# Kernel optimization log

Hardware: AMD Instinct MI355X
Metric: run time of the kernel (lower is better)

Reference implementation:

```python
import jax, jax.numpy as jnp
import numpy as np

N_NODES = 50000
N_EDGES = 800000
IN_DIM = 256
HID = 64
HEADS = 4
OUT_DIM = 16
N_GRAPHS = 64
NEG_SLOPE = 0.2


def setup_inputs() -> dict:
    key = jax.random.key(0)
    ks = jax.random.split(key, 16)
    H2 = HID // 2  # conv2 out channels (heads=1, concat=False)
    H4 = HID // 4
    inp = {
        "x": jax.random.normal(ks[0], (N_NODES, IN_DIM), jnp.float32),
        "edge_index": jax.random.randint(ks[1], (2, N_EDGES), 0, N_NODES, jnp.int64),
        "batch": jnp.sort(jax.random.randint(ks[2], (N_NODES,), 0, N_GRAPHS, jnp.int64)),
        # GATConv 1: in=IN_DIM, out=HID, heads=HEADS, concat=True
        "W1": jax.random.normal(ks[3], (IN_DIM, HEADS * HID), jnp.float32) * 0.05,
        "att_src1": jax.random.normal(ks[4], (HEADS, HID), jnp.float32) * 0.1,
        "att_dst1": jax.random.normal(ks[5], (HEADS, HID), jnp.float32) * 0.1,
        "b1": jnp.zeros((HEADS * HID,), jnp.float32),
        # GATConv 2: in=HEADS*HID, out=HID/2, heads=1, concat=False
        "W2": jax.random.normal(ks[6], (HEADS * HID, H2), jnp.float32) * 0.05,
        "att_src2": jax.random.normal(ks[7], (1, H2), jnp.float32) * 0.1,
        "att_dst2": jax.random.normal(ks[8], (1, H2), jnp.float32) * 0.1,
        "b2": jnp.zeros((H2,), jnp.float32),
        "fc1_w": jax.random.normal(ks[9], (H2, H4), jnp.float32) * 0.1,
        "fc1_b": jnp.zeros((H4,), jnp.float32),
        "fc2_w": jax.random.normal(ks[10], (H4, OUT_DIM), jnp.float32) * 0.1,
        "fc2_b": jnp.zeros((OUT_DIM,), jnp.float32),
    }
    return inp


def gat_conv(x, W, att_src, att_dst, bias, src, dst, num_nodes, concat):
    """PyG-style GATConv (eval mode, self-loops already in src/dst)."""
    H, C = att_src.shape
    h = (x @ W).reshape(num_nodes, H, C)          # [N,H,C]
    a_src = (h * att_src).sum(-1)                 # [N,H]
    a_dst = (h * att_dst).sum(-1)                 # [N,H]
    e = jax.nn.leaky_relu(a_src[src] + a_dst[dst], NEG_SLOPE)  # [E,H]
    # segment softmax over destination nodes (self-loops => every segment nonempty)
    emax = jax.ops.segment_max(e, dst, num_segments=num_nodes)
    ex = jnp.exp(e - emax[dst])
    denom = jax.ops.segment_sum(ex, dst, num_segments=num_nodes)
    alpha = ex / (denom[dst] + 1e-16)             # [E,H]
    msg = h[src] * alpha[:, :, None]              # [E,H,C]
    out = jax.ops.segment_sum(msg, dst, num_segments=num_nodes)  # [N,H,C]
    out = out.reshape(num_nodes, H * C) if concat else out.mean(axis=1)
    return out + bias


def reference(x, edge_index, batch, W1, att_src1, att_dst1, b1,
              W2, att_src2, att_dst2, b2, fc1_w, fc1_b, fc2_w, fc2_b):
    num_nodes = x.shape[0]
    loops = jnp.arange(num_nodes, dtype=edge_index.dtype)
    src = jnp.concatenate([edge_index[0], loops])
    dst = jnp.concatenate([edge_index[1], loops])

    h = gat_conv(x, W1, att_src1, att_dst1, b1, src, dst, num_nodes, concat=True)
    h = jax.nn.relu(h)                                 # dropout: eval no-op
    h = gat_conv(h, W2, att_src2, att_dst2, b2, src, dst, num_nodes, concat=False)

    # global mean pool over graphs
    sums = jax.ops.segment_sum(h, batch, num_segments=N_GRAPHS)
    cnts = jax.ops.segment_sum(jnp.ones((num_nodes,), h.dtype), batch, num_segments=N_GRAPHS)
    g = sums / jnp.maximum(cnts, 1.0)[:, None]         # [G, HID/2]

    g = jax.nn.relu(g)
    g = jax.nn.relu(g @ fc1_w + fc1_b)
    g = jax.nn.relu(g @ fc2_w + fc2_b)
    return g
```

## Files before the change

kernel.cpp:

```cpp
#include <hip/hip_runtime.h>
#include <math.h>

#define NEG 0.2f
#define LMAX 1024
#define CAP 1600
typedef unsigned short u16;
typedef unsigned int u32;
typedef __bf16 bf16x8 __attribute__((ext_vector_type(8)));
typedef float f32x4 __attribute__((ext_vector_type(4)));

__device__ __forceinline__ float bf2f(u16 u) {
    union { unsigned i; float f; } x; x.i = ((unsigned)u) << 16; return x.f;
}
__device__ __forceinline__ u16 f2bf(float f) {
    union { float f; unsigned u; } x; x.f = f;
    unsigned r = x.u + 0x7fffu + ((x.u >> 16) & 1u);
    return (u16)(r >> 16);
}

__global__ __launch_bounds__(256) void bkt_scatter_pad(const int* __restrict__ ei,
                                                       int* __restrict__ bktcur,
                                                       u32* __restrict__ ebuf,
                                                       int E, int ET, int NBK) {
    __shared__ int lcnt[LMAX];
    __shared__ int lbase[LMAX];
    int t = threadIdx.x;
    for (int b = t; b < NBK; b += 256) lcnt[b] = 0;
    __syncthreads();
    int base = blockIdx.x * 8192;
    for (int k = 0; k < 32; ++k) {
        int i = base + k * 256 + t;
        if (i < ET) {
            int d = (i < E) ? ei[E + i] : (i - E);
            atomicAdd(&lcnt[d >> 6], 1);
        }
    }
    __syncthreads();
    for (int b = t; b < NBK; b += 256) {
        int c = lcnt[b];
        lbase[b] = c ? (b * CAP + atomicAdd(&bktcur[b], c)) : 0;
    }
    __syncthreads();
    for (int b = t; b < NBK; b += 256) lcnt[b] = 0;
    __syncthreads();
    for (int k = 0; k < 32; ++k) {
        int i = base + k * 256 + t;
        if (i < ET) {
            int s, d;
            if (i < E) { s = ei[i]; d = ei[E + i]; }
            else       { s = i - E; d = s; }
            int b = d >> 6;
            int idx = atomicAdd(&lcnt[b], 1);
            ebuf[lbase[b] + idx] = (u32)s | ((u32)(d & 63) << 16);
        }
    }
}

__global__ __launch_bounds__(256) void bucket_csr_pad(const u32* __restrict__ ebuf,
                                                      const int* __restrict__ bktcur,
                                                      int* __restrict__ row_ptr,
                                                      int* __restrict__ rowend,
                                                      int* __restrict__ col, int N) {
    __shared__ int cnt[64];
    __shared__ int cur[64];
    int b = blockIdx.x, t = threadIdx.x;
    int v0 = b << 6;
    int s0 = b * CAP, s1 = s0 + bktcur[b];
    if (t < 64) cnt[t] = 0;
    __syncthreads();
    for (int i = s0 + t; i < s1; i += 256)
        atomicAdd(&cnt[(ebuf[i] >> 16) & 63], 1);
    __syncthreads();
    if (t < 64) {
        int c = cnt[t];
        int val = c;
#pragma unroll
        for (int off = 1; off < 64; off <<= 1) {
            int n = __shfl_up(val, off, 64);
            if (t >= off) val += n;
        }
        int excl = s0 + val - c;
        if (v0 + t < N) { row_ptr[v0 + t] = excl; rowend[v0 + t] = excl + c; }
        cur[t] = excl;
    }
    __syncthreads();
    for (int i = s0 + t; i < s1; i += 256) {
        u32 v = ebuf[i];
        int pos = atomicAdd(&cur[(v >> 16) & 63], 1);
        col[pos] = (int)(v & 0xFFFFu);
    }
}

__global__ void prep_all(const float* __restrict__ W1, const float* __restrict__ att_s1,
                         const float* __restrict__ att_d1, u16* __restrict__ w1x,
                         const float* __restrict__ W2, const float* __restrict__ att_s2,
                         const float* __restrict__ att_d2, u16* __restrict__ w2x,
                         int* __restrict__ bktcur, int NBK) {
    int t = threadIdx.x;
    if (blockIdx.x < 256) {
        int k = blockIdx.x;
        int c = t;
        float w = W1[k * 256 + c];
        w1x[c * 256 + k] = f2bf(w);
        int head = c >> 6;
        float vs = w * att_s1[c];
        float vd = w * att_d1[c];
#pragma unroll
        for (int mask = 1; mask < 64; mask <<= 1) {
            vs += __shfl_xor(vs, mask, 64);
            vd += __shfl_xor(vd, mask, 64);
        }
        if ((c & 63) == 0) {
            w1x[(256 + head) * 256 + k] = f2bf(vs);
            w1x[(260 + head) * 256 + k] = f2bf(vd);
            w1x[(264 + head) * 256 + k] = 0;
            w1x[(268 + head) * 256 + k] = 0;
        }
    } else {
        int k = t;
        float a_s = 0.f, a_d = 0.f;
#pragma unroll
        for (int j = 0; j < 32; ++j) {
            float w = W2[k * 32 + j];
            w2x[j * 256 + k] = f2bf(w);
            a_s += w * att_s2[j];
            a_d += w * att_d2[j];
        }
        w2x[32 * 256 + k] = f2bf(a_s);
        w2x[33 * 256 + k] = f2bf(a_d);
#pragma unroll
        for (int r = 34; r < 48; ++r) w2x[r * 256 + k] = 0;
        for (int i = t; i < NBK; i += 256) bktcur[i] = 0;
    }
}

__global__ __launch_bounds__(512) void gemm1_regw(const float* __restrict__ x,
                                                  const u16* __restrict__ w1x,
                                                  u16* __restrict__ h1b,
                                                  float* __restrict__ asad, int N) {
    __shared__ __align__(16) u16 xs[2][16][264];
    int t = threadIdx.x;
    int wave = t >> 6, lane = t & 63;
    int g = lane >> 4, l15 = lane & 15;

    bf16x8 wreg[3][8];
#pragma unroll
    for (int ci = 0; ci < 3; ++ci) {
        int ct = (ci == 2) ? 16 : (wave * 2 + ci);
        const u16* wp = w1x + (size_t)(ct * 16 + l15) * 256 + g * 8;
#pragma unroll
        for (int ks = 0; ks < 8; ++ks)
            wreg[ci][ks] = *reinterpret_cast<const bf16x8*>(wp + ks * 32);
    }

    int srow = t >> 5, sseg = t & 31;
    int ntiles = (N + 15) >> 4;
    int tile0 = blockIdx.x;
    if (tile0 >= ntiles) return;

    auto stage_load = [&](int tile, float4& a0, float4& a1) {
        int arow = tile * 16 + srow; if (arow > N - 1) arow = N - 1;
        const float* xp = x + (size_t)arow * 256 + sseg * 8;
        a0 = *reinterpret_cast<const float4*>(xp);
        a1 = *reinterpret_cast<const float4*>(xp + 4);
    };
    auto stage_write = [&](int buf, const float4& a0, const float4& a1) {
        uint4 o;
        o.x = (unsigned)f2bf(a0.x) | ((unsigned)f2bf(a0.y) << 16);
        o.y = (unsigned)f2bf(a0.z) | ((unsigned)f2bf(a0.w) << 16);
        o.z = (unsigned)f2bf(a1.x) | ((unsigned)f2bf(a1.y) << 16);
        o.w = (unsigned)f2bf(a1.z) | ((unsigned)f2bf(a1.w) << 16);
        *reinterpret_cast<uint4*>(&xs[buf][srow][sseg * 8]) = o;
    };

    {
        float4 a0, a1;
        stage_load(tile0, a0, a1);
        stage_write(0, a0, a1);
    }
    __syncthreads();

    int cur = 0;
    for (int tile = tile0; tile < ntiles; tile += 256) {
        int nxt = tile + 256;
        bool hasnext = nxt < ntiles;
        float4 p0, p1;
        if (hasnext) stage_load(nxt, p0, p1);

        f32x4 acc[3];
#pragma unroll
        for (int ci = 0; ci < 3; ++ci) acc[ci] = (f32x4){0.f, 0.f, 0.f, 0.f};
#pragma unroll
        for (int ks = 0; ks < 8; ++ks) {
            bf16x8 bfr = *reinterpret_cast<const bf16x8*>(&xs[cur][l15][ks * 32 + g * 8]);
#pragma unroll
            for (int ci = 0; ci < 3; ++ci)
                acc[ci] = __builtin_amdgcn_mfma_f32_16x16x32_bf16(wreg[ci][ks], bfr, acc[ci], 0, 0, 0);
        }

        int nrow = tile * 16 + l15;
        if (nrow < N) {
#pragma unroll
            for (int ci = 0; ci < 2; ++ci) {
                int ct = wave * 2 + ci;
                ushort4 o;
                o.x = f2bf(acc[ci][0]); o.y = f2bf(acc[ci][1]);
                o.z = f2bf(acc[ci][2]); o.w = f2bf(acc[ci][3]);
                *reinterpret_cast<ushort4*>(h1b + (size_t)nrow * 256 + ct * 16 + g * 4) = o;
            }
            if (wave == 0 && g < 2) {
#pragma unroll
                for (int reg = 0; reg < 4; ++reg)
                    asad[(size_t)nrow * 8 + g * 4 + reg] = acc[2][reg];
            }
        }
        __syncthreads();
        if (hasnext) stage_write(cur ^ 1, p0, p1);
        __syncthreads();
        cur ^= 1;
    }
}

__global__ __launch_bounds__(256) void conv1_fused(const u16* __restrict__ h1b,
                                                   const float* __restrict__ asad,
                                                   const int* __restrict__ row_ptr,
                                                   const int* __restrict__ rowend,
                                                   const int* __restrict__ col,
                                                   const float* __restrict__ b1,
                                                   u16* __restrict__ hin2b, int N) {
    __shared__ float la[4][128][4];
    __shared__ int   lc[4][128];
    int idx = blockIdx.x * blockDim.x + threadIdx.x;
    int v = idx >> 6; if (v > N - 1) v = N - 1;
    int lane = idx & 63;
    int node = threadIdx.x >> 6;
    int head = lane >> 4, l15 = lane & 15;
    float adst = asad[(size_t)v * 8 + 4 + head];
    int beg = row_ptr[v], end = rowend[v];
    int deg = end - beg;
    bool fast = (deg <= 128);
    float m = -1e30f, l = 0.f;
    if (fast) {
        float e[8]; int u[8];
#pragma unroll
        for (int i = 0; i < 8; ++i) {
            int p = beg + l15 + i * 16;
            float ev = -1e30f; int uu = 0;
            if (p < end) {
                uu = col[p];
                float tv = asad[(size_t)uu * 8 + head] + adst;
                ev = tv > 0.f ? tv : NEG * tv;
            }
            e[i] = ev; u[i] = uu;
        }
        m = e[0];
#pragma unroll
        for (int i = 1; i < 8; ++i) m = fmaxf(m, e[i]);
#pragma unroll
        for (int mask = 1; mask < 16; mask <<= 1) m = fmaxf(m, __shfl_xor(m, mask, 64));
#pragma unroll
        for (int i = 0; i < 8; ++i) {
            int j = l15 + i * 16;
            if (beg + j < end) {
                float a = __expf(e[i] - m);
                l += a;
                la[node][j][head] = a;
                if (head == 0) lc[node][j] = u[i];
            }
        }
#pragma unroll
        for (int mask = 1; mask < 16; mask <<= 1) l += __shfl_xor(l, mask, 64);
    } else {
        for (int p = beg + l15; p < end; p += 16) {
            float tv = asad[(size_t)col[p] * 8 + head] + adst;
            tv = tv > 0.f ? tv : NEG * tv;
            m = fmaxf(m, tv);
        }
#pragma unroll
        for (int mask = 1; mask < 16; mask <<= 1) m = fmaxf(m, __shfl_xor(m, mask, 64));
        for (int p = beg + l15; p < end; p += 16) {
            float tv = asad[(size_t)col[p] * 8 + head] + adst;
            tv = tv > 0.f ? tv : NEG * tv;
            l += __expf(tv - m);
        }
#pragma unroll
        for (int mask = 1; mask < 16; mask <<= 1) l += __shfl_xor(l, mask, 64);
    }
    __syncthreads();
    float inv = 1.f / (l + 1e-16f);

    float ax = 0.f, ay = 0.f, az = 0.f, aw = 0.f;
    if (fast) {
        int j = 0;
        for (; j + 3 < deg; j += 4) {
            float a0 = la[node][j + 0][head];
            float a1 = la[node][j + 1][head];
            float a2 = la[node][j + 2][head];
            float a3 = la[node][j + 3][head];
            int u0 = lc[node][j + 0], u1 = lc[node][j + 1];
            int u2 = lc[node][j + 2], u3 = lc[node][j + 3];
            ushort4 h0 = *reinterpret_cast<const ushort4*>(h1b + (size_t)u0 * 256 + lane * 4);
            ushort4 h1 = *reinterpret_cast<const ushort4*>(h1b + (size_t)u1 * 256 + lane * 4);
            ushort4 h2 = *reinterpret_cast<const ushort4*>(h1b + (size_t)u2 * 256 + lane * 4);
            ushort4 h3 = *reinterpret_cast<const ushort4*>(h1b + (size_t)u3 * 256 + lane * 4);
            ax += a0 * bf2f(h0.x) + a1 * bf2f(h1.x) + a2 * bf2f(h2.x) + a3 * bf2f(h3.x);
            ay += a0 * bf2f(h0.y) + a1 * bf2f(h1.y) + a2 * bf2f(h2.y) + a3 * bf2f(h3.y);
            az += a0 * bf2f(h0.z) + a1 * bf2f(h1.z) + a2 * bf2f(h2.z) + a3 * bf2f(h3.z);
            aw += a0 * bf2f(h0.w) + a1 * bf2f(h1.w) + a2 * bf2f(h2.w) + a3 * bf2f(h3.w);
        }
        for (; j < deg; ++j) {
            float a = la[node][j][head];
            int u = lc[node][j];
            ushort4 hv = *reinterpret_cast<const ushort4*>(h1b + (size_t)u * 256 + lane * 4);
            ax += a * bf2f(hv.x);
            ay += a * bf2f(hv.y);
            az += a * bf2f(hv.z);
            aw += a * bf2f(hv.w);
        }
    } else {
        for (int p = beg; p < end; ++p) {
            int u = col[p];
            float tv = asad[(size_t)u * 8 + head] + adst;
            tv = tv > 0.f ? tv : NEG * tv;
            float a = __expf(tv - m);
            ushort4 hv = *reinterpret_cast<const ushort4*>(h1b + (size_t)u * 256 + lane * 4);
            ax += a * bf2f(hv.x);
            ay += a * bf2f(hv.y);
            az += a * bf2f(hv.z);
            aw += a * bf2f(hv.w);
        }
    }
    int c = lane * 4;
    ushort4 o;
    o.x = f2bf(fmaxf(ax * inv + b1[c + 0], 0.f));
    o.y = f2bf(fmaxf(ay * inv + b1[c + 1], 0.f));
    o.z = f2bf(fmaxf(az * inv + b1[c + 2], 0.f));
    o.w = f2bf(fmaxf(aw * inv + b1[c + 3], 0.f));
    *reinterpret_cast<ushort4*>(hin2b + (size_t)v * 256 + c) = o;
}

__global__ __launch_bounds__(512) void gemm2_mfma(const u16* __restrict__ hin2b,
                                                  const u16* __restrict__ w2x,
                                                  u16* __restrict__ h2b,
                                                  float* __restrict__ as2,
                                                  float* __restrict__ ad2, int N) {
    __shared__ __align__(16) u16 wl[48 * 264];
    for (int f = threadIdx.x; f < 48 * 32; f += 512) {
        int r = f >> 5, cc = f & 31;
        *reinterpret_cast<uint4*>(&wl[r * 264 + cc * 8]) =
            *reinterpret_cast<const uint4*>(w2x + r * 256 + cc * 8);
    }
    __syncthreads();

    int wave = threadIdx.x >> 6, lane = threadIdx.x & 63;
    int g = lane >> 4, l15 = lane & 15;
    int ntiles = (N + 15) >> 4;
    for (int tile = blockIdx.x * 8 + wave; tile < ntiles; tile += gridDim.x * 8) {
        int r0 = tile << 4;
        int arow = r0 + l15; if (arow > N - 1) arow = N - 1;
        const u16* hp = hin2b + (size_t)arow * 256 + g * 8;

        f32x4 acc[3];
#pragma unroll
        for (int n = 0; n < 3; ++n) acc[n] = (f32x4){0.f, 0.f, 0.f, 0.f};

#pragma unroll
        for (int ks = 0; ks < 8; ++ks) {
            bf16x8 af = *reinterpret_cast<const bf16x8*>(hp + ks * 32);
#pragma unroll
            for (int n = 0; n < 3; ++n) {
                bf16x8 bf = *reinterpret_cast<const bf16x8*>(&wl[(n * 16 + l15) * 264 + ks * 32 + g * 8]);
                acc[n] = __builtin_amdgcn_mfma_f32_16x16x32_bf16(af, bf, acc[n], 0, 0, 0);
            }
        }

#pragma unroll
        for (int reg = 0; reg < 4; ++reg) {
            int grow = r0 + g * 4 + reg;
            if (grow < N) {
                h2b[(size_t)grow * 32 + l15]      = f2bf(acc[0][reg]);
                h2b[(size_t)grow * 32 + 16 + l15] = f2bf(acc[1][reg]);
                if (l15 == 0) as2[grow] = acc[2][reg];
                if (l15 == 1) ad2[grow] = acc[2][reg];
            }
        }
    }
}

__global__ __launch_bounds__(256) void conv2_fused(const u16* __restrict__ h2b,
                                                   const float* __restrict__ as2,
                                                   const float* __restrict__ ad2,
                                                   const int* __restrict__ row_ptr,
                                                   const int* __restrict__ rowend,
                                                   const int* __restrict__ col,
                                                   const float* __restrict__ b2,
                                                   float* __restrict__ out2, int N) {
    __shared__ float la[8][128];
    __shared__ int   lc[8][128];
    int idx = blockIdx.x * blockDim.x + threadIdx.x;
    int v = idx >> 5; if (v > N - 1) v = N - 1;
    int lane = idx & 31;
    int node = threadIdx.x >> 5;
    float adst = ad2[v];
    int beg = row_ptr[v], end = rowend[v];
    int deg = end - beg;
    bool fast = (deg <= 128);
    float m = -1e30f, l = 0.f;
    if (fast) {
        float e[4]; int u[4];
#pragma unroll
        for (int i = 0; i < 4; ++i) {
            int p = beg + lane + i * 32;
            float ev = -1e30f; int uu = 0;
            if (p < end) {
                uu = col[p];
                float tv = as2[uu] + adst;
                ev = tv > 0.f ? tv : NEG * tv;
            }
            e[i] = ev; u[i] = uu;
        }
        m = fmaxf(fmaxf(e[0], e[1]), fmaxf(e[2], e[3]));
#pragma unroll
        for (int mask = 1; mask < 32; mask <<= 1) m = fmaxf(m, __shfl_xor(m, mask, 64));
#pragma unroll
        for (int i = 0; i < 4; ++i) {
            int j = lane + i * 32;
            if (beg + j < end) {
                float a = __expf(e[i] - m);
                l += a;
                la[node][j] = a;
                lc[node][j] = u[i];
            }
        }
#pragma unroll
        for (int mask = 1; mask < 32; mask <<= 1) l += __shfl_xor(l, mask, 64);
    } else {
        for (int p = beg + lane; p < end; p += 32) {
            float tv = as2[col[p]] + adst;
            tv = tv > 0.f ? tv : NEG * tv;
            m = fmaxf(m, tv);
        }
#pragma unroll
        for (int mask = 1; mask < 32; mask <<= 1) m = fmaxf(m, __shfl_xor(m, mask, 64));
        for (int p = beg + lane; p < end; p += 32) {
            float tv = as2[col[p]] + adst;
            tv = tv > 0.f ? tv : NEG * tv;
            l += __expf(tv - m);
        }
#pragma unroll
        for (int mask = 1; mask < 32; mask <<= 1) l += __shfl_xor(l, mask, 64);
    }
    __syncthreads();
    float inv = 1.f / (l + 1e-16f);

    float acc = 0.f;
    if (fast) {
        int j = 0;
        for (; j + 3 < deg; j += 4) {
            float a0 = la[node][j + 0], a1 = la[node][j + 1];
            float a2 = la[node][j + 2], a3 = la[node][j + 3];
            int u0 = lc[node][j + 0], u1 = lc[node][j + 1];
            int u2 = lc[node][j + 2], u3 = lc[node][j + 3];
            acc += a0 * bf2f(h2b[(size_t)u0 * 32 + lane])
                 + a1 * bf2f(h2b[(size_t)u1 * 32 + lane])
                 + a2 * bf2f(h2b[(size_t)u2 * 32 + lane])
                 + a3 * bf2f(h2b[(size_t)u3 * 32 + lane]);
        }
        for (; j < deg; ++j)
            acc += la[node][j] * bf2f(h2b[(size_t)lc[node][j] * 32 + lane]);
    } else {
        for (int p = beg; p < end; ++p) {
            int u = col[p];
            float tv = as2[u] + adst;
            tv = tv > 0.f ? tv : NEG * tv;
            acc += __expf(tv - m) * bf2f(h2b[(size_t)u * 32 + lane]);
        }
    }
    out2[(size_t)v * 32 + lane] = acc * inv + b2[lane];
}

__global__ __launch_bounds__(256) void pool_fc(const float* __restrict__ out2,
                                               const int* __restrict__ batch,
                                               const float* __restrict__ fc1w,
                                               const float* __restrict__ fc1b,
                                               const float* __restrict__ fc2w,
                                               const float* __restrict__ fc2b,
                                               float* __restrict__ out, int N) {
    int g = blockIdx.x;
    int lo = 0, hi = N;
    while (lo < hi) { int mid = (lo + hi) >> 1; if (batch[mid] < g) lo = mid + 1; else hi = mid; }
    int s = lo;
    lo = 0; hi = N;
    while (lo < hi) { int mid = (lo + hi) >> 1; if (batch[mid] < g + 1) lo = mid + 1; else hi = mid; }
    int e = lo;

    int c = threadIdx.x & 31, grp = threadIdx.x >> 5;
    float sum = 0.f;
    for (int r = s + grp; r < e; r += 8) sum += out2[(size_t)r * 32 + c];
    __shared__ float part[8][32];
    part[grp][c] = sum;
    __syncthreads();
    __shared__ float g0[32];
    if (grp == 0) {
        float tot = 0.f;
#pragma unroll
        for (int q = 0; q < 8; ++q) tot += part[q][c];
        float cnt = (float)(e - s);
        g0[c] = fmaxf(tot / fmaxf(cnt, 1.0f), 0.f);
    }
    __syncthreads();
    __shared__ float z1[16];
    if (threadIdx.x < 16) {
        float a = fc1b[threadIdx.x];
        for (int k = 0; k < 32; ++k) a += g0[k] * fc1w[k * 16 + threadIdx.x];
        z1[threadIdx.x] = fmaxf(a, 0.f);
    }
    __syncthreads();
    if (threadIdx.x < 16) {
        float a = fc2b[threadIdx.x];
        for (int k = 0; k < 16; ++k) a += z1[k] * fc2w[k * 16 + threadIdx.x];
        out[g * 16 + threadIdx.x] = fmaxf(a, 0.f);
    }
}

extern "C" void kernel_launch(void* const* d_in, const int* in_sizes, int n_in,
                              void* d_out, int out_size, void* d_ws, size_t ws_size,
                              hipStream_t stream) {
    const float* x      = (const float*)d_in[0];
    const int*   ei     = (const int*)d_in[1];
    const int*   batch  = (const int*)d_in[2];
    const float* W1     = (const float*)d_in[3];
    const float* att_s1 = (const float*)d_in[4];
    const float* att_d1 = (const float*)d_in[5];
    const float* b1     = (const float*)d_in[6];
    const float* W2     = (const float*)d_in[7];
    const float* att_s2 = (const float*)d_in[8];
    const float* att_d2 = (const float*)d_in[9];
    const float* b2     = (const float*)d_in[10];
    const float* fc1w   = (const float*)d_in[11];
    const float* fc1b   = (const float*)d_in[12];
    const float* fc2w   = (const float*)d_in[13];
    const float* fc2b   = (const float*)d_in[14];
    float* out = (float*)d_out;

    int N = in_sizes[0] / 256;
    int E = in_sizes[1] / 2;
    int ET = E + N;
    int NBK = (N + 63) >> 6;
    int nchunks = (ET + 8191) / 8192;

    char* ws = (char*)d_ws;
    size_t off = 0;
    auto alloc = [&](size_t bytes) { size_t o = off; off = (off + bytes + 255) & ~255ULL; return o; };
    u16*  w1x    = (u16*)(ws + alloc(272 * 256 * 2));
    u16*  w2x    = (u16*)(ws + alloc(48 * 256 * 2));
    u16*  h1b    = (u16*)(ws + alloc((size_t)N * 256 * 2));
    float* asad  = (float*)(ws + alloc((size_t)N * 8 * 4));
    u16*  hin2b  = (u16*)(ws + alloc((size_t)N * 256 * 2));
    u16*  h2b    = (u16*)(ws + alloc((size_t)N * 32 * 2));
    float* as2   = (float*)(ws + alloc((size_t)N * 4));
    float* ad2   = (float*)(ws + alloc((size_t)N * 4));
    float* out2  = (float*)(ws + alloc((size_t)N * 32 * 4));
    int* row_ptr = (int*)(ws + alloc((size_t)N * 4));
    int* rowend  = (int*)(ws + alloc((size_t)N * 4));
    int* col     = (int*)(ws + alloc((size_t)NBK * CAP * 4));
    int* bktcur  = (int*)(ws + alloc((size_t)NBK * 4));
    u32* ebuf    = (u32*)(ws + alloc((size_t)NBK * CAP * 4));
    (void)ws_size; (void)n_in; (void)out_size;

    prep_all<<<257, 256, 0, stream>>>(W1, att_s1, att_d1, w1x, W2, att_s2, att_d2, w2x, bktcur, NBK);

    bkt_scatter_pad<<<nchunks, 256, 0, stream>>>(ei, bktcur, ebuf, E, ET, NBK);
    bucket_csr_pad<<<NBK, 256, 0, stream>>>(ebuf, bktcur, row_ptr, rowend, col, N);

    gemm1_regw<<<256, 512, 0, stream>>>(x, w1x, h1b, asad, N);
    conv1_fused<<<(N * 64 + 255) / 256, 256, 0, stream>>>(h1b, asad, row_ptr, rowend, col, b1, hin2b, N);

    gemm2_mfma<<<256, 512, 0, stream>>>(hin2b, w2x, h2b, as2, ad2, N);
    conv2_fused<<<(N * 32 + 255) / 256, 256, 0, stream>>>(h2b, as2, ad2, row_ptr, rowend, col, b2, out2, N);

    pool_fc<<<64, 256, 0, stream>>>(out2, batch, fc1w, fc1b, fc2w, fc2b, out, N);
}
```

Measured before the change: 196.4 us.

## Fuse edge bucket scatter into GEMM1 launch via block specialization

Merges the edge bucket-scatter kernel into the first GEMM kernel, with extra blocks beyond the first 256 doing the scatter, so the two independent stages run concurrently and one launch is removed. The scatter chunk size drops from 8192 to 2048 edges per block to give more parallel scatter blocks using 512 threads. The cost is more global atomics on bucket counters and larger shared memory per block, which may lower GEMM occupancy.

```diff
diff --git a/kernel.cpp b/kernel.cpp
--- a/kernel.cpp
+++ b/kernel.cpp
@@ -4,6 +4,7 @@
 #define NEG 0.2f
 #define LMAX 1024
 #define CAP 1600
+#define SCHUNK 2048
 typedef unsigned short u16;
 typedef unsigned int u32;
 typedef __bf16 bf16x8 __attribute__((ext_vector_type(8)));
@@ -16,79 +17,6 @@
     union { float f; unsigned u; } x; x.f = f;
     unsigned r = x.u + 0x7fffu + ((x.u >> 16) & 1u);
     return (u16)(r >> 16);
-}
-
-__global__ __launch_bounds__(256) void bkt_scatter_pad(const int* __restrict__ ei,
-                                                       int* __restrict__ bktcur,
-                                                       u32* __restrict__ ebuf,
-                                                       int E, int ET, int NBK) {
-    __shared__ int lcnt[LMAX];
-    __shared__ int lbase[LMAX];
-    int t = threadIdx.x;
-    for (int b = t; b < NBK; b += 256) lcnt[b] = 0;
-    __syncthreads();
-    int base = blockIdx.x * 8192;
-    for (int k = 0; k < 32; ++k) {
-        int i = base + k * 256 + t;
-        if (i < ET) {
-            int d = (i < E) ? ei[E + i] : (i - E);
-            atomicAdd(&lcnt[d >> 6], 1);
-        }
-    }
-    __syncthreads();
-    for (int b = t; b < NBK; b += 256) {
-        int c = lcnt[b];
-        lbase[b] = c ? (b * CAP + atomicAdd(&bktcur[b], c)) : 0;
-    }
-    __syncthreads();
-    for (int b = t; b < NBK; b += 256) lcnt[b] = 0;
-    __syncthreads();
-    for (int k = 0; k < 32; ++k) {
-        int i = base + k * 256 + t;
-        if (i < ET) {
-            int s, d;
-            if (i < E) { s = ei[i]; d = ei[E + i]; }
-            else       { s = i - E; d = s; }
-            int b = d >> 6;
-            int idx = atomicAdd(&lcnt[b], 1);
-            ebuf[lbase[b] + idx] = (u32)s | ((u32)(d & 63) << 16);
-        }
-    }
-}
-
-__global__ __launch_bounds__(256) void bucket_csr_pad(const u32* __restrict__ ebuf,
-                                                      const int* __restrict__ bktcur,
-                                                      int* __restrict__ row_ptr,
-                                                      int* __restrict__ rowend,
-                                                      int* __restrict__ col, int N) {
-    __shared__ int cnt[64];
-    __shared__ int cur[64];
-    int b = blockIdx.x, t = threadIdx.x;
-    int v0 = b << 6;
-    int s0 = b * CAP, s1 = s0 + bktcur[b];
-    if (t < 64) cnt[t] = 0;
-    __syncthreads();
-    for (int i = s0 + t; i < s1; i += 256)
-        atomicAdd(&cnt[(ebuf[i] >> 16) & 63], 1);
-    __syncthreads();
-    if (t < 64) {
-        int c = cnt[t];
-        int val = c;
-#pragma unroll
-        for (int off = 1; off < 64; off <<= 1) {
-            int n = __shfl_up(val, off, 64);
-            if (t >= off) val += n;
-        }
-        int excl = s0 + val - c;
-        if (v0 + t < N) { row_ptr[v0 + t] = excl; rowend[v0 + t] = excl + c; }
-        cur[t] = excl;
-    }
-    __syncthreads();
-    for (int i = s0 + t; i < s1; i += 256) {
-        u32 v = ebuf[i];
-        int pos = atomicAdd(&cur[(v >> 16) & 63], 1);
-        col[pos] = (int)(v & 0xFFFFu);
-    }
 }
 
 __global__ void prep_all(const float* __restrict__ W1, const float* __restrict__ att_s1,
@@ -134,90 +62,164 @@
     }
 }
 
-__global__ __launch_bounds__(512) void gemm1_regw(const float* __restrict__ x,
-                                                  const u16* __restrict__ w1x,
-                                                  u16* __restrict__ h1b,
-                                                  float* __restrict__ asad, int N) {
+__global__ __launch_bounds__(512) void gemm1_and_scatter(
+        const float* __restrict__ x, const u16* __restrict__ w1x,
+        u16* __restrict__ h1b, float* __restrict__ asad, int N,
+        const int* __restrict__ ei, int* __restrict__ bktcur,
+        u32* __restrict__ ebuf, int E, int ET, int NBK) {
     __shared__ __align__(16) u16 xs[2][16][264];
+    __shared__ int lcnt[LMAX];
+    __shared__ int lbase[LMAX];
     int t = threadIdx.x;
-    int wave = t >> 6, lane = t & 63;
-    int g = lane >> 4, l15 = lane & 15;
-
-    bf16x8 wreg[3][8];
-#pragma unroll
-    for (int ci = 0; ci < 3; ++ci) {
-        int ct = (ci == 2) ? 16 : (wave * 2 + ci);
-        const u16* wp = w1x + (size_t)(ct * 16 + l15) * 256 + g * 8;
-#pragma unroll
-        for (int ks = 0; ks < 8; ++ks)
-            wreg[ci][ks] = *reinterpret_cast<const bf16x8*>(wp + ks * 32);
-    }
-
-    int srow = t >> 5, sseg = t & 31;
-    int ntiles = (N + 15) >> 4;
-    int tile0 = blockIdx.x;
-    if (tile0 >= ntiles) return;
-
-    auto stage_load = [&](int tile, float4& a0, float4& a1) {
-        int arow = tile * 16 + srow; if (arow > N - 1) arow = N - 1;
-        const float* xp = x + (size_t)arow * 256 + sseg * 8;
-        a0 = *reinterpret_cast<const float4*>(xp);
-        a1 = *reinterpret_cast<const float4*>(xp + 4);
-    };
-    auto stage_write = [&](int buf, const float4& a0, const float4& a1) {
-        uint4 o;
-        o.x = (unsigned)f2bf(a0.x) | ((unsigned)f2bf(a0.y) << 16);
-        o.y = (unsigned)f2bf(a0.z) | ((unsigned)f2bf(a0.w) << 16);
-        o.z = (unsigned)f2bf(a1.x) | ((unsigned)f2bf(a1.y) << 16);
-        o.w = (unsigned)f2bf(a1.z) | ((unsigned)f2bf(a1.w) << 16);
-        *reinterpret_cast<uint4*>(&xs[buf][srow][sseg * 8]) = o;
-    };
-
-    {
-        float4 a0, a1;
-        stage_load(tile0, a0, a1);
-        stage_write(0, a0, a1);
-    }
-    __syncthreads();
-
-    int cur = 0;
-    for (int tile = tile0; tile < ntiles; tile += 256) {
-        int nxt = tile + 256;
-        bool hasnext = nxt < ntiles;
-        float4 p0, p1;
-        if (hasnext) stage_load(nxt, p0, p1);
-
-        f32x4 acc[3];
-#pragma unroll
-        for (int ci = 0; ci < 3; ++ci) acc[ci] = (f32x4){0.f, 0.f, 0.f, 0.f};
-#pragma unroll
-        for (int ks = 0; ks < 8; ++ks) {
-            bf16x8 bfr = *reinterpret_cast<const bf16x8*>(&xs[cur][l15][ks * 32 + g * 8]);
-#pragma unroll
-            for (int ci = 0; ci < 3; ++ci)
-                acc[ci] = __builtin_amdgcn_mfma_f32_16x16x32_bf16(wreg[ci][ks], bfr, acc[ci], 0, 0, 0);
-        }
-
-        int nrow = tile * 16 + l15;
-        if (nrow < N) {
-#pragma unroll
-            for (int ci = 0; ci < 2; ++ci) {
-                int ct = wave * 2 + ci;
-                ushort4 o;
-                o.x = f2bf(acc[ci][0]); o.y = f2bf(acc[ci][1]);
-                o.z = f2bf(acc[ci][2]); o.w = f2bf(acc[ci][3]);
-                *reinterpret_cast<ushort4*>(h1b + (size_t)nrow * 256 + ct * 16 + g * 4) = o;
-            }
-            if (wave == 0 && g < 2) {
-#pragma unroll
-                for (int reg = 0; reg < 4; ++reg)
-                    asad[(size_t)nrow * 8 + g * 4 + reg] = acc[2][reg];
-            }
+
+    if (blockIdx.x < 256) {
+        int wave = t >> 6, lane = t & 63;
+        int g = lane >> 4, l15 = lane & 15;
+
+        bf16x8 wreg[3][8];
+#pragma unroll
+        for (int ci = 0; ci < 3; ++ci) {
+            int ct = (ci == 2) ? 16 : (wave * 2 + ci);
+            const u16* wp = w1x + (size_t)(ct * 16 + l15) * 256 + g * 8;
+#pragma unroll
+            for (int ks = 0; ks < 8; ++ks)
+                wreg[ci][ks] = *reinterpret_cast<const bf16x8*>(wp + ks * 32);
+        }
+
+        int srow = t >> 5, sseg = t & 31;
+        int ntiles = (N + 15) >> 4;
+        int tile0 = blockIdx.x;
+        if (tile0 >= ntiles) return;
+
+        auto stage_load = [&](int tile, float4& a0, float4& a1) {
+            int arow = tile * 16 + srow; if (arow > N - 1) arow = N - 1;
+            const float* xp = x + (size_t)arow * 256 + sseg * 8;
+            a0 = *reinterpret_cast<const float4*>(xp);
+            a1 = *reinterpret_cast<const float4*>(xp + 4);
+        };
+        auto stage_write = [&](int buf, const float4& a0, const float4& a1) {
+            uint4 o;
+            o.x = (unsigned)f2bf(a0.x) | ((unsigned)f2bf(a0.y) << 16);
+            o.y = (unsigned)f2bf(a0.z) | ((unsigned)f2bf(a0.w) << 16);
+            o.z = (unsigned)f2bf(a1.x) | ((unsigned)f2bf(a1.y) << 16);
+            o.w = (unsigned)f2bf(a1.z) | ((unsigned)f2bf(a1.w) << 16);
+            *reinterpret_cast<uint4*>(&xs[buf][srow][sseg * 8]) = o;
+        };
+
+        {
+            float4 a0, a1;
+            stage_load(tile0, a0, a1);
+            stage_write(0, a0, a1);
         }
         __syncthreads();
-        if (hasnext) stage_write(cur ^ 1, p0, p1);
+
+        int cur = 0;
+        for (int tile = tile0; tile < ntiles; tile += 256) {
+            int nxt = tile + 256;
+            bool hasnext = nxt < ntiles;
+            float4 p0, p1;
+            if (hasnext) stage_load(nxt, p0, p1);
+
+            f32x4 acc[3];
+#pragma unroll
+            for (int ci = 0; ci < 3; ++ci) acc[ci] = (f32x4){0.f, 0.f, 0.f, 0.f};
+#pragma unroll
+            for (int ks = 0; ks < 8; ++ks) {
+                bf16x8 bfr = *reinterpret_cast<const bf16x8*>(&xs[cur][l15][ks * 32 + g * 8]);
+#pragma unroll
+                for (int ci = 0; ci < 3; ++ci)
+                    acc[ci] = __builtin_amdgcn_mfma_f32_16x16x32_bf16(wreg[ci][ks], bfr, acc[ci], 0, 0, 0);
+            }
+
+            int nrow = tile * 16 + l15;
+            if (nrow < N) {
+#pragma unroll
+                for (int ci = 0; ci < 2; ++ci) {
+                    int ct = wave * 2 + ci;
+                    ushort4 o;
+                    o.x = f2bf(acc[ci][0]); o.y = f2bf(acc[ci][1]);
+                    o.z = f2bf(acc[ci][2]); o.w = f2bf(acc[ci][3]);
+                    *reinterpret_cast<ushort4*>(h1b + (size_t)nrow * 256 + ct * 16 + g * 4) = o;
+                }
+                if (wave == 0 && g < 2) {
+#pragma unroll
+                    for (int reg = 0; reg < 4; ++reg)
+                        asad[(size_t)nrow * 8 + g * 4 + reg] = acc[2][reg];
+                }
+            }
+            __syncthreads();
+            if (hasnext) stage_write(cur ^ 1, p0, p1);
+            __syncthreads();
+            cur ^= 1;
+        }
+    } else {
+        int cb = blockIdx.x - 256;
+        for (int b = t; b < NBK; b += 512) lcnt[b] = 0;
         __syncthreads();
-        cur ^= 1;
+        int base = cb * SCHUNK;
+#pragma unroll
+        for (int k = 0; k < SCHUNK / 512; ++k) {
+            int i = base + k * 512 + t;
+            if (i < ET) {
+                int d = (i < E) ? ei[E + i] : (i - E);
+                atomicAdd(&lcnt[d >> 6], 1);
+            }
+        }
+        __syncthreads();
+        for (int b = t; b < NBK; b += 512) {
+            int c = lcnt[b];
+            lbase[b] = c ? (b * CAP + atomicAdd(&bktcur[b], c)) : 0;
+        }
+        __syncthreads();
+        for (int b = t; b < NBK; b += 512) lcnt[b] = 0;
+        __syncthreads();
+#pragma unroll
+        for (int k = 0; k < SCHUNK / 512; ++k) {
+            int i = base + k * 512 + t;
+            if (i < ET) {
+                int s, d;
+                if (i < E) { s = ei[i]; d = ei[E + i]; }
+                else       { s = i - E; d = s; }
+                int b = d >> 6;
+                int idx = atomicAdd(&lcnt[b], 1);
+                ebuf[lbase[b] + idx] = (u32)s | ((u32)(d & 63) << 16);
+            }
+        }
+    }
+}
+
+__global__ __launch_bounds__(256) void bucket_csr_pad(const u32* __restrict__ ebuf,
+                                                      const int* __restrict__ bktcur,
+                                                      int* __restrict__ row_ptr,
+                                                      int* __restrict__ rowend,
+                                                      int* __restrict__ col, int N) {
+    __shared__ int cnt[64];
+    __shared__ int cur[64];
+    int b = blockIdx.x, t = threadIdx.x;
+    int v0 = b << 6;
+    int s0 = b * CAP, s1 = s0 + bktcur[b];
+    if (t < 64) cnt[t] = 0;
+    __syncthreads();
+    for (int i = s0 + t; i < s1; i += 256)
+        atomicAdd(&cnt[(ebuf[i] >> 16) & 63], 1);
+    __syncthreads();
+    if (t < 64) {
+        int c = cnt[t];
+        int val = c;
+#pragma unroll
+        for (int off = 1; off < 64; off <<= 1) {
+            int n = __shfl_up(val, off, 64);
+            if (t >= off) val += n;
+        }
+        int excl = s0 + val - c;
+        if (v0 + t < N) { row_ptr[v0 + t] = excl; rowend[v0 + t] = excl + c; }
+        cur[t] = excl;
+    }
+    __syncthreads();
+    for (int i = s0 + t; i < s1; i += 256) {
+        u32 v = ebuf[i];
+        int pos = atomicAdd(&cur[(v >> 16) & 63], 1);
+        col[pos] = (int)(v & 0xFFFFu);
     }
 }
 
@@ -547,7 +549,7 @@
     int E = in_sizes[1] / 2;
     int ET = E + N;
     int NBK = (N + 63) >> 6;
-    int nchunks = (ET + 8191) / 8192;
+    int nchunks = (ET + SCHUNK - 1) / SCHUNK;
 
     char* ws = (char*)d_ws;
     size_t off = 0;
@@ -570,10 +572,11 @@
 
     prep_all<<<257, 256, 0, stream>>>(W1, att_s1, att_d1, w1x, W2, att_s2, att_d2, w2x, bktcur, NBK);
 
-    bkt_scatter_pad<<<nchunks, 256, 0, stream>>>(ei, bktcur, ebuf, E, ET, NBK);
+    gemm1_and_scatter<<<256 + nchunks, 512, 0, stream>>>(x, w1x, h1b, asad, N,
+                                                         ei, bktcur, ebuf, E, ET, NBK);
+
     bucket_csr_pad<<<NBK, 256, 0, stream>>>(ebuf, bktcur, row_ptr, rowend, col, N);
 
-    gemm1_regw<<<256, 512, 0, stream>>>(x, w1x, h1b, asad, N);
     conv1_fused<<<(N * 64 + 255) / 256, 256, 0, stream>>>(h1b, asad, row_ptr, rowend, col, b1, hin2b, N);
 
     gemm2_mfma<<<256, 512, 0, stream>>>(hin2b, w2x, h2b, as2, ad2, N);
```

New measurement: 181.3 us, median of 2. 7.7% less time.
